# Kernel tuning notes

Hardware: AMD Instinct MI355X
Metric: run time of the kernel (lower is better)

The kernel has to match this reference:

```python
import jax, jax.numpy as jnp
import numpy as np


def _orthogonalize(Wfree):
    # Wfree: (S, C, C) free parameters -> batched QR with sign correction
    Q, R = jnp.linalg.qr(Wfree)
    s = jnp.sign(jnp.diagonal(R, axis1=-2, axis2=-1))  # (S, C)
    s = jnp.where(s == 0, jnp.ones_like(s), s)
    return Q * s[:, None, :]  # column-wise sign fix


def _channel_mix(x, Wfree):
    # x: (B, C, H, W); Wfree: (H*W, C, C)
    B, C, H, Wd = x.shape
    S = H * Wd
    Q = _orthogonalize(Wfree)                      # (S, C, C)
    xr = x.reshape(B, C, S).transpose(0, 2, 1)     # (B, S, C)
    # y[b,s,:] = x[b,s,:] @ Q[s].T  (matches torch matmul(x, Q.T))
    y = jnp.einsum('bsk,sck->bsc', xr, Q)
    return y.transpose(0, 2, 1).reshape(B, C, H, Wd)


def setup_inputs() -> dict:
    key = jax.random.key(0)
    k0, k1, k2, k3 = jax.random.split(key, 4)
    init_scale = 0.001
    x0 = jax.random.normal(k0, (32, 64, 28, 28), dtype=jnp.float32)
    x1 = jax.random.normal(k1, (32, 256, 14, 14), dtype=jnp.float32)
    W0 = jax.random.normal(k2, (28 * 28, 64, 64), dtype=jnp.float32) * init_scale
    W1 = jax.random.normal(k3, (14 * 14, 256, 256), dtype=jnp.float32) * init_scale
    return {"x0": x0, "x1": x1, "W0": W0, "W1": W1}


def reference(x0, x1, W0, W1):
    # C=64 and C=256 are perfect squares, so channel padding is a no-op.
    y0 = _channel_mix(x0, W0)
    y1 = _channel_mix(x1, W1)
    return (y0, y1)
```

## Files before the change

kernel.cpp:

```cpp
#include <hip/hip_runtime.h>


static constexpr int BB = 32;

#define SCHED_FENCE() __builtin_amdgcn_sched_barrier(0)

template<int CTRL>
__device__ __forceinline__ float dpp_add(float x) {
    int y = __builtin_amdgcn_update_dpp(0, __float_as_int(x), CTRL, 0xF, 0xF, false);
    return x + __int_as_float(y);
}
__device__ __forceinline__ float rowred16(float p) {
    p = dpp_add<0x128>(p);
    p = dpp_add<0x124>(p);
    p = dpp_add<0x122>(p);
    p = dpp_add<0x121>(p);
    return p;
}

__device__ __forceinline__ int qoff(int j, int g, int r16) {
    return j * 256 + g * 64 + ((r16 ^ (2 * g)) << 2);
}

__global__ __launch_bounds__(256) void tkern(const float* __restrict__ in,
                                             float* __restrict__ out,
                                             int R, int S) {
    __shared__ float tile[32][33];
    const int tx = threadIdx.x, ty = threadIdx.y;
    const int s0 = blockIdx.x * 32, r0 = blockIdx.y * 32;
    #pragma unroll
    for (int i = ty; i < 32; i += 8) {
        int r = r0 + i, s = s0 + tx;
        tile[i][tx] = (r < R && s < S) ? in[(size_t)r * S + s] : 0.f;
    }
    __syncthreads();
    #pragma unroll
    for (int i = ty; i < 32; i += 8) {
        int s = s0 + i, r = r0 + tx;
        if (s < S && r < R) out[(size_t)s * R + r] = tile[tx][i];
    }
}

template<int C, int CT, int KC>
__device__ __forceinline__ void qr_body(const float* __restrict__ W,
                                        float* __restrict__ XY,
                                        float* __restrict__ sm, int t) {
    constexpr int RT = 16;
    constexpr int TR = C / RT;
    constexpr int THREADS = RT * CT;
    constexpr int QSTR = TR + 4;
    constexpr int XSTR = C + 4;

    float* qs = sm;
    float* xs = sm + 2 * RT * QSTR;
    float* qc = xs + BB * XSTR;

    const int rb = t & 15;
    const int cb = t >> 4;

    float a[TR][4];
    {
        const float* Wp = W + (size_t)(rb * TR) * C + cb * 4;
        #pragma unroll
        for (int i = 0; i < TR; ++i) {
            float4 v = *reinterpret_cast<const float4*>(Wp + (size_t)i * C);
            a[i][0] = v.x; a[i][1] = v.y; a[i][2] = v.z; a[i][3] = v.w;
        }
    }
    {
        #pragma unroll
        for (int v = 0; v < (BB * C) / (4 * THREADS); ++v) {
            int idx = 4 * (t + v * THREADS);
            int b = idx / C, k = idx % C;
            float4 x4 = *reinterpret_cast<const float4*>(XY + idx);
            *reinterpret_cast<float4*>(&xs[b * XSTR + k]) = x4;
        }
    }

    int buf = 0;
    #pragma unroll 1
    for (int j = 0; j < C; ++j) {
        const int cbj = j >> 2, jj = j & 3;
        if (cb == cbj) {
            #pragma unroll
            for (int q = 0; q < 4; ++q) {
                if (q == jj) {
                    float p = 0.f;
                    #pragma unroll
                    for (int i = 0; i < TR; ++i) p += a[i][q] * a[i][q];
                    p = rowred16(p);
                    const float rn = 1.0f / sqrtf(p);
                    #pragma unroll
                    for (int i = 0; i < TR; ++i) a[i][q] *= rn;
                    #pragma unroll
                    for (int i = 0; i < TR; i += 4) {
                        *reinterpret_cast<float4*>(&qs[buf * RT * QSTR + rb * QSTR + i]) =
                            make_float4(a[i][q], a[i+1][q], a[i+2][q], a[i+3][q]);
                    }
                }
            }
        }
        __syncthreads();
        if (cb * 4 + 3 > j) {
            float qv[TR];
            #pragma unroll
            for (int i = 0; i < TR; i += 4) {
                float4 v = *reinterpret_cast<const float4*>(&qs[buf * RT * QSTR + rb * QSTR + i]);
                qv[i] = v.x; qv[i+1] = v.y; qv[i+2] = v.z; qv[i+3] = v.w;
            }
            #pragma unroll
            for (int q = 0; q < 4; ++q) {
                if (cb * 4 + q > j) {
                    float p = 0.f;
                    #pragma unroll
                    for (int i = 0; i < TR; ++i) p += a[i][q] * qv[i];
                    p = rowred16(p);
                    #pragma unroll
                    for (int i = 0; i < TR; ++i) a[i][q] -= p * qv[i];
                }
            }
        }
        buf ^= 1;
    }

    const int u  = t % (C / 4);
    const int bp = t / (C / 4);
    float acc[2][4] = {{0,0,0,0},{0,0,0,0}};

    #pragma unroll 1
    for (int ch = 0; ch < C / KC; ++ch) {
        __syncthreads();
        if (cb >= (ch * KC) / 4 && cb < ((ch + 1) * KC) / 4) {
            #pragma unroll
            for (int q = 0; q < 4; ++q) {
                const int kk = cb * 4 + q - ch * KC;
                const int swz = (kk & 7) << 2;
                #pragma unroll
                for (int i = 0; i < TR; i += 4) {
                    const int cout = rb * TR + i;
                    *reinterpret_cast<float4*>(&qc[kk * C + (cout ^ swz)]) =
                        make_float4(a[i][q], a[i+1][q], a[i+2][q], a[i+3][q]);
                }
            }
        }
        __syncthreads();
        #pragma unroll
        for (int kk = 0; kk < KC; kk += 4) {
            const int k = ch * KC + kk;
            float4 x0 = *reinterpret_cast<const float4*>(&xs[(2*bp    ) * XSTR + k]);
            float4 x1 = *reinterpret_cast<const float4*>(&xs[(2*bp + 1) * XSTR + k]);
            #pragma unroll
            for (int m = 0; m < 4; ++m) {
                const int swz = ((kk + m) & 7) << 2;
                float4 qv4 = *reinterpret_cast<const float4*>(&qc[(kk + m) * C + ((4 * u) ^ swz)]);
                const float xa = (&x0.x)[m], xb = (&x1.x)[m];
                acc[0][0] += xa * qv4.x; acc[0][1] += xa * qv4.y;
                acc[0][2] += xa * qv4.z; acc[0][3] += xa * qv4.w;
                acc[1][0] += xb * qv4.x; acc[1][1] += xb * qv4.y;
                acc[1][2] += xb * qv4.z; acc[1][3] += xb * qv4.w;
            }
        }
    }
    {
        *reinterpret_cast<float4*>(XY + (2*bp    ) * C + 4 * u) =
            make_float4(acc[0][0], acc[0][1], acc[0][2], acc[0][3]);
        *reinterpret_cast<float4*>(XY + (2*bp + 1) * C + 4 * u) =
            make_float4(acc[1][0], acc[1][1], acc[1][2], acc[1][3]);
    }
}

__device__ __forceinline__ void dot_upd(float (&a)[2][16], const float* qpan,
                                        int j, int rb) {
    const float4 q40 = *reinterpret_cast<const float4*>(&qpan[qoff(j, 0, rb)]);
    const float4 q41 = *reinterpret_cast<const float4*>(&qpan[qoff(j, 1, rb)]);
    const float4 q42 = *reinterpret_cast<const float4*>(&qpan[qoff(j, 2, rb)]);
    const float4 q43 = *reinterpret_cast<const float4*>(&qpan[qoff(j, 3, rb)]);
    float p0 = 0.f, p1 = 0.f;
    p0 += a[0][ 0]*q40.x; p1 += a[1][ 0]*q40.x;
    p0 += a[0][ 1]*q40.y; p1 += a[1][ 1]*q40.y;
    p0 += a[0][ 2]*q40.z; p1 += a[1][ 2]*q40.z;
    p0 += a[0][ 3]*q40.w; p1 += a[1][ 3]*q40.w;
    p0 += a[0][ 4]*q41.x; p1 += a[1][ 4]*q41.x;
    p0 += a[0][ 5]*q41.y; p1 += a[1][ 5]*q41.y;
    p0 += a[0][ 6]*q41.z; p1 += a[1][ 6]*q41.z;
    p0 += a[0][ 7]*q41.w; p1 += a[1][ 7]*q41.w;
    p0 += a[0][ 8]*q42.x; p1 += a[1][ 8]*q42.x;
    p0 += a[0][ 9]*q42.y; p1 += a[1][ 9]*q42.y;
    p0 += a[0][10]*q42.z; p1 += a[1][10]*q42.z;
    p0 += a[0][11]*q42.w; p1 += a[1][11]*q42.w;
    p0 += a[0][12]*q43.x; p1 += a[1][12]*q43.x;
    p0 += a[0][13]*q43.y; p1 += a[1][13]*q43.y;
    p0 += a[0][14]*q43.z; p1 += a[1][14]*q43.z;
    p0 += a[0][15]*q43.w; p1 += a[1][15]*q43.w;
    p0 = rowred16(p0); p1 = rowred16(p1);
    a[0][ 0] -= p0*q40.x; a[0][ 1] -= p0*q40.y;
    a[0][ 2] -= p0*q40.z; a[0][ 3] -= p0*q40.w;
    a[0][ 4] -= p0*q41.x; a[0][ 5] -= p0*q41.y;
    a[0][ 6] -= p0*q41.z; a[0][ 7] -= p0*q41.w;
    a[0][ 8] -= p0*q42.x; a[0][ 9] -= p0*q42.y;
    a[0][10] -= p0*q42.z; a[0][11] -= p0*q42.w;
    a[0][12] -= p0*q43.x; a[0][13] -= p0*q43.y;
    a[0][14] -= p0*q43.z; a[0][15] -= p0*q43.w;
    a[1][ 0] -= p1*q40.x; a[1][ 1] -= p1*q40.y;
    a[1][ 2] -= p1*q40.z; a[1][ 3] -= p1*q40.w;
    a[1][ 4] -= p1*q41.x; a[1][ 5] -= p1*q41.y;
    a[1][ 6] -= p1*q41.z; a[1][ 7] -= p1*q41.w;
    a[1][ 8] -= p1*q42.x; a[1][ 9] -= p1*q42.y;
    a[1][10] -= p1*q42.z; a[1][11] -= p1*q42.w;
    a[1][12] -= p1*q43.x; a[1][13] -= p1*q43.y;
    a[1][14] -= p1*q43.z; a[1][15] -= p1*q43.w;
}

__device__ __forceinline__ void mini_mgs2(float (&a)[2][16], float* qpan,
                                          int jx, int rb) {
    float p = 0.f;
    #pragma unroll
    for (int i = 0; i < 16; ++i) p += a[0][i] * a[0][i];
    p = rowred16(p);
    float rn = 1.0f / sqrtf(p);
    #pragma unroll
    for (int i = 0; i < 16; ++i) a[0][i] *= rn;
    #pragma unroll
    for (int g = 0; g < 4; ++g) {
        *reinterpret_cast<float4*>(&qpan[qoff(jx, g, rb)]) =
            make_float4(a[0][4*g], a[0][4*g+1], a[0][4*g+2], a[0][4*g+3]);
    }
    float q = 0.f;
    #pragma unroll
    for (int i = 0; i < 16; ++i) q += a[1][i] * a[0][i];
    q = rowred16(q);
    #pragma unroll
    for (int i = 0; i < 16; ++i) a[1][i] -= q * a[0][i];
    p = 0.f;
    #pragma unroll
    for (int i = 0; i < 16; ++i) p += a[1][i] * a[1][i];
    p = rowred16(p);
    rn = 1.0f / sqrtf(p);
    #pragma unroll
    for (int i = 0; i < 16; ++i) a[1][i] *= rn;
    #pragma unroll
    for (int g = 0; g < 4; ++g) {
        *reinterpret_cast<float4*>(&qpan[qoff(jx + 1, g, rb)]) =
            make_float4(a[1][4*g], a[1][4*g+1], a[1][4*g+2], a[1][4*g+3]);
    }
}

__device__ __forceinline__ void apply1(float (&y0)[4], float (&y1)[4],
                                       const float* qpan, const float* xsb,
                                       int j, int u, int v) {
    float4 q4 = *reinterpret_cast<const float4*>(&qpan[qoff(j, u & 3, u >> 2)]);
    const float xa = xsb[j*33 + 2*v];
    const float xb = xsb[j*33 + 2*v + 1];
    y0[0] += xa*q4.x; y0[1] += xa*q4.y; y0[2] += xa*q4.z; y0[3] += xa*q4.w;
    y1[0] += xb*q4.x; y1[1] += xb*q4.y; y1[2] += xb*q4.z; y1[3] += xb*q4.w;
}

__device__ void panel_mgs(float (&a)[2][16], float (&y0)[4], float (&y1)[4],
                          float* qpan, const float* xsb,
                          int rb, int cb, int u, int v) {
    if (cb == 0) mini_mgs2(a, qpan, 0, rb);
    __syncthreads();
    #pragma unroll 1
    for (int m = 0; m < 64; ++m) {
        apply1(y0, y1, qpan, xsb, 2*m,     u, v);
        apply1(y0, y1, qpan, xsb, 2*m + 1, u, v);
        SCHED_FENCE();
        if (cb > m) {
            dot_upd(a, qpan, 2*m,     rb);
            SCHED_FENCE();
            dot_upd(a, qpan, 2*m + 1, rb);
            SCHED_FENCE();
            if (cb == m + 1) mini_mgs2(a, qpan, 2*m + 2, rb);
        }
        __syncthreads();
    }
}

__device__ __forceinline__ void qr256_site(const float* __restrict__ Wp,
                                           float* __restrict__ Xp,
                                           float* __restrict__ sm, int t) {
    float* qpan = sm;
    float* xsb  = sm + 32768;

    const int rb = t & 15;
    const int cb = t >> 4;
    const int u  = t & 63;
    const int v  = t >> 6;

    float a[2][16];
    float y0[4] = {0,0,0,0};
    float y1[4] = {0,0,0,0};

    #pragma unroll
    for (int i = 0; i < 16; ++i) {
        float2 w2 = *reinterpret_cast<const float2*>(
            Wp + (size_t)(rb*16 + i) * 256 + 2*cb);
        a[0][i] = w2.x; a[1][i] = w2.y;
    }
    {
        const int tj = t & 127, tb = t >> 7;
        #pragma unroll
        for (int d = 0; d < 4; ++d)
            xsb[tj*33 + 4*tb + d] = Xp[(4*tb + d)*256 + tj];
    }
    panel_mgs(a, y0, y1, qpan, xsb, rb, cb, u, v);

    __syncthreads();
    #pragma unroll
    for (int i = 0; i < 16; ++i) {
        float2 w2 = *reinterpret_cast<const float2*>(
            Wp + (size_t)(rb*16 + i) * 256 + 128 + 2*cb);
        a[0][i] = w2.x; a[1][i] = w2.y;
    }
    {
        const int tj = t & 127, tb = t >> 7;
        #pragma unroll
        for (int d = 0; d < 4; ++d)
            xsb[tj*33 + 4*tb + d] = Xp[(4*tb + d)*256 + 128 + tj];
    }
    #pragma unroll 1
    for (int k = 0; k < 128; ++k) {
        dot_upd(a, qpan, k, rb);
        SCHED_FENCE();
    }
    __syncthreads();

    panel_mgs(a, y0, y1, qpan, xsb, rb, cb, u, v);

    *reinterpret_cast<float4*>(Xp + (size_t)(2*v    )*256 + 4*u) =
        make_float4(y0[0], y0[1], y0[2], y0[3]);
    *reinterpret_cast<float4*>(Xp + (size_t)(2*v + 1)*256 + 4*u) =
        make_float4(y1[0], y1[1], y1[2], y1[3]);
}

static constexpr int SM64 = 2*16*8 + 32*68 + 64*64;

__global__ __launch_bounds__(1024) void qr_all(const float* __restrict__ W0,
                                               const float* __restrict__ W1,
                                               float* __restrict__ XY0,
                                               float* __restrict__ XY1) {
    __shared__ float sm[32768 + 128*33];
    const int bid = blockIdx.x;
    const int t   = threadIdx.x;
    if (bid < 196) {
        qr256_site(W1 + (size_t)bid * 65536, XY1 + (size_t)bid * 8192, sm, t);
    } else {
        const int sl = t >> 8;
        const int tt = t & 255;
        float* smL = sm + sl * SM64;
        #pragma unroll 1
        for (int uu = bid - 196; uu < 196; uu += 60) {
            const int site = 4 * uu + sl;
            qr_body<64, 16, 64>(W0 + (size_t)site * 4096,
                                XY0 + (size_t)site * 2048, smL, tt);
            __syncthreads();
        }
    }
}

extern "C" void kernel_launch(void* const* d_in, const int* in_sizes, int n_in,
                              void* d_out, int out_size, void* d_ws, size_t ws_size,
                              hipStream_t stream) {
    (void)in_sizes; (void)n_in; (void)out_size; (void)ws_size;
    const float* x0 = (const float*)d_in[0];
    const float* x1 = (const float*)d_in[1];
    const float* W0 = (const float*)d_in[2];
    const float* W1 = (const float*)d_in[3];
    float* y0  = (float*)d_out;
    float* y1  = y0 + 1605632;
    float* xt0 = (float*)d_ws;
    float* xt1 = xt0 + 1605632;

    dim3 tb(32, 8);
    tkern<<<dim3(25,  64), tb, 0, stream>>>(x0, xt0, 2048, 784);
    tkern<<<dim3(7,  256), tb, 0, stream>>>(x1, xt1, 8192, 196);
    qr_all<<<256, 1024, 0, stream>>>(W0, W1, xt0, xt1);
    tkern<<<dim3(64,  25), tb, 0, stream>>>(xt0, y0, 784, 2048);
    tkern<<<dim3(256,  7), tb, 0, stream>>>(xt1, y1, 196, 8192);
}
```

Baseline: 250.1 us.

## Move Q application out of the MGS panel loop and transpose the x staging

The Q·x accumulation was interleaved with each Gram-Schmidt step inside the 128-column panel loop. It now runs as a separate pass after each panel is fully orthogonalized. The staged x block is stored transposed with a row stride of 132, so each thread loads four x values per float4 instead of scalar reads. The panel loop also drops the final iteration, which only did apply work and a barrier. This removes per-step apply work and LDS traffic from the serial MGS critical path, but gives up hiding that work behind the idle threads of each barrier step.

```diff
diff --git a/kernel.cpp b/kernel.cpp
--- a/kernel.cpp
+++ b/kernel.cpp
@@ -245,26 +245,11 @@
     }
 }
 
-__device__ __forceinline__ void apply1(float (&y0)[4], float (&y1)[4],
-                                       const float* qpan, const float* xsb,
-                                       int j, int u, int v) {
-    float4 q4 = *reinterpret_cast<const float4*>(&qpan[qoff(j, u & 3, u >> 2)]);
-    const float xa = xsb[j*33 + 2*v];
-    const float xb = xsb[j*33 + 2*v + 1];
-    y0[0] += xa*q4.x; y0[1] += xa*q4.y; y0[2] += xa*q4.z; y0[3] += xa*q4.w;
-    y1[0] += xb*q4.x; y1[1] += xb*q4.y; y1[2] += xb*q4.z; y1[3] += xb*q4.w;
-}
-
-__device__ void panel_mgs(float (&a)[2][16], float (&y0)[4], float (&y1)[4],
-                          float* qpan, const float* xsb,
-                          int rb, int cb, int u, int v) {
+__device__ void panel_mgs(float (&a)[2][16], float* qpan, int rb, int cb) {
     if (cb == 0) mini_mgs2(a, qpan, 0, rb);
     __syncthreads();
     #pragma unroll 1
-    for (int m = 0; m < 64; ++m) {
-        apply1(y0, y1, qpan, xsb, 2*m,     u, v);
-        apply1(y0, y1, qpan, xsb, 2*m + 1, u, v);
-        SCHED_FENCE();
+    for (int m = 0; m < 63; ++m) {
         if (cb > m) {
             dot_upd(a, qpan, 2*m,     rb);
             SCHED_FENCE();
@@ -276,6 +261,26 @@
     }
 }
 
+static constexpr int XST2 = 132;
+
+__device__ __forceinline__ void apply_panel(float (&y0)[4], float (&y1)[4],
+                                            const float* qpan, const float* xsb,
+                                            int u, int v) {
+    #pragma unroll 1
+    for (int j4 = 0; j4 < 128; j4 += 4) {
+        float4 xa4 = *reinterpret_cast<const float4*>(&xsb[(2*v    ) * XST2 + j4]);
+        float4 xb4 = *reinterpret_cast<const float4*>(&xsb[(2*v + 1) * XST2 + j4]);
+        #pragma unroll
+        for (int m = 0; m < 4; ++m) {
+            const int j = j4 + m;
+            float4 q4 = *reinterpret_cast<const float4*>(&qpan[qoff(j, u & 3, u >> 2)]);
+            const float xa = (&xa4.x)[m], xb = (&xb4.x)[m];
+            y0[0] += xa*q4.x; y0[1] += xa*q4.y; y0[2] += xa*q4.z; y0[3] += xa*q4.w;
+            y1[0] += xb*q4.x; y1[1] += xb*q4.y; y1[2] += xb*q4.z; y1[3] += xb*q4.w;
+        }
+    }
+}
+
 __device__ __forceinline__ void qr256_site(const float* __restrict__ Wp,
                                            float* __restrict__ Xp,
                                            float* __restrict__ sm, int t) {
@@ -297,26 +302,28 @@
             Wp + (size_t)(rb*16 + i) * 256 + 2*cb);
         a[0][i] = w2.x; a[1][i] = w2.y;
     }
-    {
-        const int tj = t & 127, tb = t >> 7;
-        #pragma unroll
-        for (int d = 0; d < 4; ++d)
-            xsb[tj*33 + 4*tb + d] = Xp[(4*tb + d)*256 + tj];
-    }
-    panel_mgs(a, y0, y1, qpan, xsb, rb, cb, u, v);
-
+    #pragma unroll
+    for (int p = 0; p < 4; ++p) {
+        const int idx = t + p * 1024;
+        const int b = idx >> 7, jj = idx & 127;
+        xsb[b * XST2 + jj] = Xp[b * 256 + jj];
+    }
+    panel_mgs(a, qpan, rb, cb);
+
+    apply_panel(y0, y1, qpan, xsb, u, v);
     __syncthreads();
+
     #pragma unroll
     for (int i = 0; i < 16; ++i) {
         float2 w2 = *reinterpret_cast<const float2*>(
             Wp + (size_t)(rb*16 + i) * 256 + 128 + 2*cb);
         a[0][i] = w2.x; a[1][i] = w2.y;
     }
-    {
-        const int tj = t & 127, tb = t >> 7;
-        #pragma unroll
-        for (int d = 0; d < 4; ++d)
-            xsb[tj*33 + 4*tb + d] = Xp[(4*tb + d)*256 + 128 + tj];
+    #pragma unroll
+    for (int p = 0; p < 4; ++p) {
+        const int idx = t + p * 1024;
+        const int b = idx >> 7, jj = idx & 127;
+        xsb[b * XST2 + jj] = Xp[b * 256 + 128 + jj];
     }
     #pragma unroll 1
     for (int k = 0; k < 128; ++k) {
@@ -325,7 +332,8 @@
     }
     __syncthreads();
 
-    panel_mgs(a, y0, y1, qpan, xsb, rb, cb, u, v);
+    panel_mgs(a, qpan, rb, cb);
+    apply_panel(y0, y1, qpan, xsb, u, v);
 
     *reinterpret_cast<float4*>(Xp + (size_t)(2*v    )*256 + 4*u) =
         make_float4(y0[0], y0[1], y0[2], y0[3]);
@@ -339,7 +347,7 @@
                                                const float* __restrict__ W1,
                                                float* __restrict__ XY0,
                                                float* __restrict__ XY1) {
-    __shared__ float sm[32768 + 128*33];
+    __shared__ float sm[32768 + 32 * XST2];
     const int bid = blockIdx.x;
     const int t   = threadIdx.x;
     if (bid < 196) {
```

Result: no change. 253.6 us (+1.4%).
